# Performance work log

Measured on AMD Instinct MI355X. Metric: run time of the kernel, lower is better.

The kernel has to match this reference:

```python
import jax, jax.numpy as jnp
import numpy as np
from functools import partial

EMB = 768
ATTN = 768
HEADS = 12
N = 4096
K = 64
ALPHA = 0.5
TEMP = 0.5
THRESH = 1e-4
MAX_ITER = 100
DKM_EPS = 1e-6
LN_EPS = 1e-5


def setup_inputs() -> dict:
    key = jax.random.key(0)
    ks = jax.random.split(key, 12)
    s = 0.02
    return {
        "original_embeddings": jax.random.normal(ks[0], (N, EMB), jnp.float32),
        "fc1_w": jax.random.normal(ks[1], (ATTN, EMB), jnp.float32) * s,
        "fc1_b": jnp.zeros((ATTN,), jnp.float32),
        "fc2_w": jax.random.normal(ks[2], (EMB, ATTN), jnp.float32) * s,
        "fc2_b": jnp.zeros((EMB,), jnp.float32),
        "in_proj_w": jax.random.normal(ks[3], (3 * ATTN, ATTN), jnp.float32) * s,
        "in_proj_b": jnp.zeros((3 * ATTN,), jnp.float32),
        "out_w": jax.random.normal(ks[4], (ATTN, ATTN), jnp.float32) * s,
        "out_b": jnp.zeros((ATTN,), jnp.float32),
        "ln_g": jnp.ones((EMB,), jnp.float32),
        "ln_b": jnp.zeros((EMB,), jnp.float32),
        "init_idx": jax.random.randint(ks[5], (K,), 0, N, jnp.int64 if jax.config.jax_enable_x64 else jnp.int32),
        "k_cl": K,
    }


def _cdist(x, c):
    # squared euclidean via expansion, clipped for numerical safety
    sq = (jnp.sum(x * x, 1)[:, None] + jnp.sum(c * c, 1)[None, :]
          - 2.0 * (x @ c.T))
    return jnp.sqrt(jnp.maximum(sq, 0.0))


def _dkm_step(X, C):
    a = jax.nn.softmax(-_cdist(X, C) / TEMP, axis=1)   # [N, K]
    a_sum = jnp.sum(a, axis=0) + DKM_EPS               # [K]
    C_new = (a.T @ X) / a_sum[:, None]                 # [K, D]
    return a, C_new


def _transform(x, fc1_w, fc1_b, fc2_w, fc2_b, in_proj_w, in_proj_b, out_w, out_b, ln_g, ln_b):
    h = jax.nn.relu(x @ fc1_w.T + fc1_b)               # [N, A]
    qkv = h @ in_proj_w.T + in_proj_b                  # [N, 3A]
    q, k, v = jnp.split(qkv, 3, axis=1)
    hd = ATTN // HEADS
    q = q.reshape(N, HEADS, hd).transpose(1, 0, 2)     # [H, N, hd]
    k = k.reshape(N, HEADS, hd).transpose(1, 0, 2)
    v = v.reshape(N, HEADS, hd).transpose(1, 0, 2)
    scores = jnp.einsum('hnd,hmd->hnm', q, k) / np.sqrt(hd).astype(np.float32)
    attn = jax.nn.softmax(scores, axis=-1)             # [H, N, N]
    o = jnp.einsum('hnm,hmd->hnd', attn, v)            # [H, N, hd]
    o = o.transpose(1, 0, 2).reshape(N, ATTN)
    o = o @ out_w.T + out_b
    y = jax.nn.relu(o @ fc2_w.T + fc2_b)               # [N, E]
    z = (1.0 - ALPHA) * x + ALPHA * y
    mu = jnp.mean(z, axis=-1, keepdims=True)
    var = jnp.mean((z - mu) ** 2, axis=-1, keepdims=True)
    return (z - mu) / jnp.sqrt(var + LN_EPS) * ln_g + ln_b


def reference(original_embeddings, fc1_w, fc1_b, fc2_w, fc2_b,
              in_proj_w, in_proj_b, out_w, out_b, ln_g, ln_b,
              init_idx, k_cl):
    X = _transform(original_embeddings, fc1_w, fc1_b, fc2_w, fc2_b,
                   in_proj_w, in_proj_b, out_w, out_b, ln_g, ln_b)
    C0 = X[init_idx]                                   # [K, E]
    a0, C1 = _dkm_step(X, C0)
    diff0 = jnp.sum(jnp.abs(C1 - C0))

    def cond(st):
        _, _, _, diff, i = st
        return (diff > THRESH) & (i < MAX_ITER)

    def body(st):
        _, _, C_new, _, i = st
        C = C_new
        a, C_new2 = _dkm_step(X, C)
        diff = jnp.sum(jnp.abs(C_new2 - C))
        return (C, a, C_new2, diff, i + 1)

    C, a, _, _, _ = jax.lax.while_loop(cond, body, (C0, a0, C1, diff0, jnp.int32(0)))
    return C, a
```

## Files before the change

kernel.cpp:

```cpp
#include <hip/hip_runtime.h>
#include <cstdint>

typedef __bf16 bf16;
typedef __bf16 bf16x4 __attribute__((ext_vector_type(4)));
typedef __bf16 bf16x8 __attribute__((ext_vector_type(8)));
typedef float  f32x4  __attribute__((ext_vector_type(4)));

#define LOG2E 1.44269504088896340736f

__device__ __forceinline__ f32x4 mfma16(bf16x8 a, bf16x8 b, f32x4 c) {
  return __builtin_amdgcn_mfma_f32_16x16x32_bf16(a, b, c, 0, 0, 0);
}

__device__ __forceinline__ void gl2lds16(const bf16* g, bf16* l) {
  __builtin_amdgcn_global_load_lds(
      (const __attribute__((address_space(1))) unsigned int*)g,
      (__attribute__((address_space(3))) unsigned int*)l, 16, 0, 0);
}

__global__ __launch_bounds__(256) void cvt_all(
    const float* __restrict__ x0, const float* __restrict__ w1,
    const float* __restrict__ w2, const float* __restrict__ wip,
    const float* __restrict__ wo,
    bf16* __restrict__ dx0, bf16* __restrict__ dw1, bf16* __restrict__ dw2,
    bf16* __restrict__ dwip, bf16* __restrict__ dwo, float* __restrict__ ctrl)
{
  int i = blockIdx.x * 256 + threadIdx.x;
  if (blockIdx.x == 0) {
    for (int u = threadIdx.x; u < 8192; u += 256) ctrl[u] = 0.f;
  }
  const float* s; bf16* d; int base;
  if      (i <  786432) { s = x0;  d = dx0;  base = 0; }
  else if (i <  933888) { s = w1;  d = dw1;  base = 786432; }
  else if (i < 1081344) { s = w2;  d = dw2;  base = 933888; }
  else if (i < 1523712) { s = wip; d = dwip; base = 1081344; }
  else                  { s = wo;  d = dwo;  base = 1523712; }
  int j = i - base;
  f32x4 v = ((const f32x4*)s)[j];
  bf16x4 r;
  r[0] = (bf16)v[0]; r[1] = (bf16)v[1]; r[2] = (bf16)v[2]; r[3] = (bf16)v[3];
  ((bf16x4*)d)[j] = r;
}

__global__ __launch_bounds__(256) void bias_fuse(
    const float* __restrict__ w2, const float* __restrict__ bo,
    const float* __restrict__ b2, float* __restrict__ bc)
{
  const int w = threadIdx.x >> 6, lane = threadIdx.x & 63;
  const int n = blockIdx.x * 4 + w;
  float s = 0.f;
#pragma unroll
  for (int i = 0; i < 12; ++i) {
    int col = lane + i * 64;
    s += w2[(size_t)n * 768 + col] * bo[col];
  }
#pragma unroll
  for (int off = 32; off; off >>= 1) s += __shfl_xor(s, off, 64);
  if (lane == 0) bc[n] = b2[n] + s;
}

template<int RELU, int OUTF32>
__global__ __launch_bounds__(256) void gemm128(
    const bf16* __restrict__ A, const bf16* __restrict__ W,
    const float* __restrict__ bias, bf16* __restrict__ outb,
    float* __restrict__ outf, int N)
{
  __shared__ bf16 Ab[2][8192];
  __shared__ bf16 Bb[2][8192];
  const int tid = threadIdx.x;
  const int w = tid >> 6, lane = tid & 63;
  const int q2 = lane >> 4, c = lane & 15;
  const int wrow = (w >> 1) * 64, wcol = (w & 1) * 64;
  const int mb = blockIdx.x * 128, nb = blockIdx.y * 128;
  const int srow = tid >> 3, sgrp = tid & 7;

  auto stage = [&](const bf16* __restrict__ src, int rowbase, int kb, bf16* dst) {
#pragma unroll
    for (int i = 0; i < 4; ++i) {
      int row = i * 32 + srow;
      int gs = (sgrp ^ (row & 7)) * 8;
      gl2lds16(src + (size_t)(rowbase + row) * 768 + kb + gs,
               dst + i * 2048 + tid * 8);
    }
  };

  f32x4 acc[4][4] = {};
  stage(A, mb, 0, Ab[0]);
  stage(W, nb, 0, Bb[0]);
  for (int kb = 0; kb < 12; ++kb) {
    const int buf = kb & 1;
    __syncthreads();
    if (kb < 11) {
      stage(A, mb, (kb + 1) * 64, Ab[buf ^ 1]);
      stage(W, nb, (kb + 1) * 64, Bb[buf ^ 1]);
    }
#pragma unroll
    for (int kc = 0; kc < 2; ++kc) {
      bf16x8 af[4], bfr[4];
#pragma unroll
      for (int rt = 0; rt < 4; ++rt) {
        int r = wrow + rt * 16 + c;
        af[rt] = *(const bf16x8*)&Ab[buf][r * 64 + (((kc * 4 + q2) ^ (r & 7)) * 8)];
      }
#pragma unroll
      for (int ct = 0; ct < 4; ++ct) {
        int r = wcol + ct * 16 + c;
        bfr[ct] = *(const bf16x8*)&Bb[buf][r * 64 + (((kc * 4 + q2) ^ (r & 7)) * 8)];
      }
#pragma unroll
      for (int rt = 0; rt < 4; ++rt)
#pragma unroll
        for (int ct = 0; ct < 4; ++ct)
          acc[rt][ct] = mfma16(af[rt], bfr[ct], acc[rt][ct]);
    }
  }
#pragma unroll
  for (int rt = 0; rt < 4; ++rt) {
#pragma unroll
    for (int ct = 0; ct < 4; ++ct) {
      int col = nb + wcol + ct * 16 + c;
      float bv = bias[col];
#pragma unroll
      for (int j = 0; j < 4; ++j) {
        int row = mb + wrow + rt * 16 + q2 * 4 + j;
        float v = acc[rt][ct][j] + bv;
        if (RELU) v = fmaxf(v, 0.f);
        if (OUTF32) outf[(size_t)row * N + col] = v;
        else        outb[(size_t)row * N + col] = (bf16)v;
      }
    }
  }
}

__global__ __launch_bounds__(256) void transpose_bf16(
    const bf16* __restrict__ src, bf16* __restrict__ dst,
    int stride, int colOff, int dstride)
{
  __shared__ bf16 t[64][72];
  const int br = blockIdx.x, bc = blockIdx.y;
  {
    int ir = threadIdx.x >> 2, icb = (threadIdx.x & 3) * 16;
    const bf16* srow = src + (size_t)(br * 64 + ir) * stride + colOff + bc * 64 + icb;
    *(bf16x8*)&t[ir][icb] = *(const bf16x8*)srow;
    *(bf16x8*)&t[ir][icb + 8] = *(const bf16x8*)(srow + 8);
  }
  __syncthreads();
  {
    int oc = threadIdx.x >> 2, orb = (threadIdx.x & 3) * 16;
    bf16x8 v0, v1;
#pragma unroll
    for (int j = 0; j < 8; ++j) { v0[j] = t[orb + j][oc]; v1[j] = t[orb + 8 + j][oc]; }
    bf16* drow = dst + (size_t)(bc * 64 + oc) * dstride + br * 64 + orb;
    *(bf16x8*)drow = v0;
    *(bf16x8*)(drow + 8) = v1;
  }
}

__global__ __launch_bounds__(256) void attn_kernel(
    const bf16* __restrict__ qkv, const bf16* __restrict__ vt, bf16* __restrict__ o)
{
  const int h = blockIdx.x >> 6;
  const int qt = blockIdx.x & 63;
  const int w = threadIdx.x >> 6, lane = threadIdx.x & 63;
  const int q2 = lane >> 4, c = lane & 15;
  const int qbase = qt * 64 + w * 16;
  __shared__ bf16 Ks[2][64][64];
  __shared__ bf16 Vs[2][64][64];
  __shared__ bf16 Pl[4][16][72];

  const bf16* Qr = qkv + (size_t)(qbase + c) * 2304 + h * 64 + q2 * 8;
  bf16x8 a0 = *(const bf16x8*)(Qr);
  bf16x8 a1 = *(const bf16x8*)(Qr + 32);

  const int srow = lane >> 3;
  const int sg = ((lane & 7) ^ srow) * 8;
  const bf16* kg = qkv + (size_t)(w * 16 + srow) * 2304 + 768 + h * 64 + sg;
  const bf16* vg = vt + (size_t)(h * 64 + w * 16 + srow) * 4096 + sg;

  auto stage = [&](int jt, int buf) {
    const int kvb = jt * 64;
    gl2lds16(kg + (size_t)kvb * 2304,       &Ks[buf][w * 16][0]);
    gl2lds16(kg + (size_t)(kvb + 8) * 2304, &Ks[buf][w * 16 + 8][0]);
    gl2lds16(vg + kvb,                      &Vs[buf][w * 16][0]);
    gl2lds16(vg + kvb + 8 * 4096,           &Vs[buf][w * 16 + 8][0]);
  };

  bf16x8 ones;
#pragma unroll
  for (int i = 0; i < 8; ++i) ones[i] = (bf16)1.0f;

  f32x4 oa[4] = {};
  f32x4 accl = {};
  const int gsw = (q2 ^ (c & 7)) * 8;
  const float SC = 0.125f * LOG2E;

  stage(0, 0);
  for (int jt = 0; jt < 64; ++jt) {
    const int buf = jt & 1;
    __syncthreads();
    if (jt < 63) stage(jt + 1, buf ^ 1);
    f32x4 s[4];
#pragma unroll
    for (int nt = 0; nt < 4; ++nt) {
      const int row = nt * 16 + c;
      bf16x8 b0 = *(const bf16x8*)&Ks[buf][row][gsw];
      bf16x8 b1 = *(const bf16x8*)&Ks[buf][row][gsw ^ 32];
      f32x4 t = {};
      t = mfma16(a0, b0, t);
      t = mfma16(a1, b1, t);
      s[nt] = t;
    }
#pragma unroll
    for (int nt = 0; nt < 4; ++nt)
#pragma unroll
      for (int j = 0; j < 4; ++j)
        Pl[w][q2 * 4 + j][nt * 16 + c] = (bf16)exp2f(s[nt][j] * SC);
    bf16x8 p0 = *(const bf16x8*)(&Pl[w][c][q2 * 8]);
    bf16x8 p1 = *(const bf16x8*)(&Pl[w][c][32 + q2 * 8]);
    accl = mfma16(p0, ones, accl);
    accl = mfma16(p1, ones, accl);
#pragma unroll
    for (int dt = 0; dt < 4; ++dt) {
      const int row = dt * 16 + c;
      bf16x8 v0 = *(const bf16x8*)&Vs[buf][row][gsw];
      bf16x8 v1 = *(const bf16x8*)&Vs[buf][row][gsw ^ 32];
      oa[dt] = mfma16(p0, v0, oa[dt]);
      oa[dt] = mfma16(p1, v1, oa[dt]);
    }
  }
#pragma unroll
  for (int dt = 0; dt < 4; ++dt)
#pragma unroll
    for (int j = 0; j < 4; ++j) {
      int row = qbase + q2 * 4 + j;
      int col = h * 64 + dt * 16 + c;
      o[(size_t)row * 768 + col] = (bf16)(oa[dt][j] / accl[j]);
    }
}

__global__ __launch_bounds__(256) void ln_kernel(
    const float* __restrict__ x0, const float* __restrict__ y,
    const float* __restrict__ g, const float* __restrict__ b,
    float* __restrict__ X, bf16* __restrict__ Xb, float* __restrict__ xn2)
{
  const int w = threadIdx.x >> 6, lane = threadIdx.x & 63;
  const int row = blockIdx.x * 4 + w;
  const float* xr = x0 + (size_t)row * 768;
  const float* yr = y + (size_t)row * 768;
  float z[12]; float s = 0.f;
#pragma unroll
  for (int i = 0; i < 12; ++i) {
    int col = lane + i * 64;
    float zz = 0.5f * xr[col] + 0.5f * yr[col];
    z[i] = zz; s += zz;
  }
#pragma unroll
  for (int off = 32; off; off >>= 1) s += __shfl_xor(s, off, 64);
  float mu = s * (1.f / 768.f);
  float v = 0.f;
#pragma unroll
  for (int i = 0; i < 12; ++i) { float d = z[i] - mu; v += d * d; }
#pragma unroll
  for (int off = 32; off; off >>= 1) v += __shfl_xor(v, off, 64);
  float rstd = rsqrtf(v * (1.f / 768.f) + 1e-5f);
  float sn = 0.f;
#pragma unroll
  for (int i = 0; i < 12; ++i) {
    int col = lane + i * 64;
    float xv = (z[i] - mu) * rstd * g[col] + b[col];
    X[(size_t)row * 768 + col] = xv;
    Xb[(size_t)row * 768 + col] = (bf16)xv;
    sn += xv * xv;
  }
#pragma unroll
  for (int off = 32; off; off >>= 1) sn += __shfl_xor(sn, off, 64);
  if (lane == 0) xn2[row] = sn;
}

__device__ __forceinline__ void gridbar(int* bar, int& ep, int g) {
  __syncthreads();
  if (threadIdx.x == 0) {
    ep++;
    __builtin_amdgcn_fence(__ATOMIC_RELEASE, "agent");
    int v = __hip_atomic_fetch_add(bar + g * 64, 1, __ATOMIC_RELAXED,
                                   __HIP_MEMORY_SCOPE_AGENT) + 1;
    if (v == 32 * ep) {
      int tv = __hip_atomic_fetch_add(bar + 512, 1, __ATOMIC_RELAXED,
                                      __HIP_MEMORY_SCOPE_AGENT) + 1;
      if (tv == 8 * ep) {
#pragma unroll
        for (int i = 0; i < 8; ++i)
          __hip_atomic_store(bar + 1024 + i * 64, ep, __ATOMIC_RELAXED,
                             __HIP_MEMORY_SCOPE_AGENT);
      }
    }
    long guard = 0;
    while (__hip_atomic_load(bar + 1024 + g * 64, __ATOMIC_RELAXED,
                             __HIP_MEMORY_SCOPE_AGENT) < ep) {
      __builtin_amdgcn_s_sleep(2);
      if (++guard > (1L << 28)) break;
    }
    __builtin_amdgcn_fence(__ATOMIC_ACQUIRE, "agent");
  }
  __syncthreads();
}

__global__ __launch_bounds__(256) void dkm_fused(
    const float* __restrict__ XF, const int* __restrict__ idx,
    const bf16* __restrict__ Xb, const bf16* __restrict__ Xt,
    const float* __restrict__ xn2,
    float* __restrict__ CB, bf16* __restrict__ CBH,
    bf16* __restrict__ aT, float* __restrict__ a_out, float* __restrict__ outC,
    float* __restrict__ asumall, float* __restrict__ cnall,
    float* __restrict__ diffall, int* __restrict__ bar)
{
  extern __shared__ char dynsmem[];
  bf16* XtL = (bf16*)dynsmem;
  __shared__ bf16 XL[16][776];
  __shared__ float GsRed[1024];
  __shared__ float asl[64];
  __shared__ float cnl[16];
  __shared__ float dred[4];
  __shared__ float sdiff;
  float (*Gs)[64] = (float(*)[64])GsRed;
  float (*red)[16][16] = (float(*)[16][16])GsRed;
  const int tid = threadIdx.x;
  const int w = tid >> 6, lane = tid & 63;
  const int q2 = lane >> 4, c = lane & 15;
  const int b = blockIdx.x;
  const int g = b & 7;
  const int rbase = b * 16;
  const int tr = b / 48, tc = b % 48;
  int ep = 0;

  {
    int row = tid >> 4, seg = (tid & 15) * 48;
    const bf16* src = Xb + (size_t)(rbase + row) * 768 + seg;
#pragma unroll
    for (int i = 0; i < 6; ++i)
      *(bf16x8*)&XL[row][seg + i * 8] = *(const bf16x8*)(src + i * 8);
  }
  if (b < 192) {
    const int row = tid >> 4, cc = tid & 15;
    const bf16* XtS = Xt + (size_t)(tc * 16 + row) * 4096;
#pragma unroll
    for (int i = 0; i < 32; ++i) {
      int gg = i * 16 + cc;
      bf16x8 vv = *(const bf16x8*)(XtS + gg * 8);
      *(bf16x8*)&XtL[(size_t)row * 4096 + ((gg ^ (row & 7)) * 8)] = vv;
    }
  }
  if (b < 64) {
    const int src = idx[b];
    float s = 0.f;
#pragma unroll
    for (int u = 0; u < 3; ++u) {
      int d = u * 256 + tid;
      float v = XF[(size_t)src * 768 + d];
      CB[(size_t)b * 768 + d] = v;
      CBH[(size_t)b * 768 + d] = (bf16)v;
      s += v * v;
    }
#pragma unroll
    for (int off = 32; off; off >>= 1) s += __shfl_xor(s, off, 64);
    if (lane == 0) dred[w] = s;
    __syncthreads();
    if (tid == 0) cnall[b] = dred[0] + dred[1] + dred[2] + dred[3];
  }
  const int arow = tid >> 4, aci = tid & 15;
  const float xn = xn2[rbase + arow];
  gridbar(bar, ep, g);

  int p = 0;
  for (int t = 0; t < 100; ++t) {
    const int par = t & 1;
    {
      if (b == 0) {
        if (tid >= 128 && tid < 192) asumall[(par ^ 1) * 64 + tid - 128] = 0.f;
        else if (tid >= 192)         cnall[(par ^ 1) * 64 + tid - 192] = 0.f;
      }
      const bf16* C = CBH + (size_t)par * 49152;
      const float* cnp = cnall + par * 64;
      const bf16* Cr = C + (size_t)(w * 16 + c) * 768 + q2 * 8;
      f32x4 a0 = {}, a1 = {}, a2 = {}, a3 = {};
#pragma unroll
      for (int ks = 0; ks < 24; ks += 4) {
        a0 = mfma16(*(const bf16x8*)&XL[c][q2 * 8 + ks * 32],
                    *(const bf16x8*)(Cr + ks * 32), a0);
        a1 = mfma16(*(const bf16x8*)&XL[c][q2 * 8 + (ks + 1) * 32],
                    *(const bf16x8*)(Cr + (ks + 1) * 32), a1);
        a2 = mfma16(*(const bf16x8*)&XL[c][q2 * 8 + (ks + 2) * 32],
                    *(const bf16x8*)(Cr + (ks + 2) * 32), a2);
        a3 = mfma16(*(const bf16x8*)&XL[c][q2 * 8 + (ks + 3) * 32],
                    *(const bf16x8*)(Cr + (ks + 3) * 32), a3);
      }
      f32x4 acc = (a0 + a1) + (a2 + a3);
      if (tid < 64) asl[tid] = 0.f;
#pragma unroll
      for (int j = 0; j < 4; ++j) Gs[q2 * 4 + j][w * 16 + c] = acc[j];
      __syncthreads();
      float lg[4];
#pragma unroll
      for (int u = 0; u < 4; ++u) {
        int col = aci + u * 16;
        float d2 = xn + cnp[col] - 2.f * Gs[arow][col];
        lg[u] = -2.f * sqrtf(fmaxf(d2, 0.f));
      }
      float mx = fmaxf(fmaxf(lg[0], lg[1]), fmaxf(lg[2], lg[3]));
#pragma unroll
      for (int off = 8; off; off >>= 1) mx = fmaxf(mx, __shfl_xor(mx, off, 16));
      float sum = 0.f;
#pragma unroll
      for (int u = 0; u < 4; ++u) { float e = exp2f((lg[u] - mx) * LOG2E); lg[u] = e; sum += e; }
#pragma unroll
      for (int off = 8; off; off >>= 1) sum += __shfl_xor(sum, off, 16);
      float rs = 1.f / sum;
#pragma unroll
      for (int u = 0; u < 4; ++u) {
        int col = aci + u * 16;
        float av = lg[u] * rs;
        aT[(size_t)col * 4096 + rbase + arow] = (bf16)av;
        atomicAdd(&asl[col], av);
      }
      __syncthreads();
      if (tid < 64) atomicAdd(&asumall[par * 64 + tid], asl[tid]);
    }
    gridbar(bar, ep, g);
    if (b < 192) {
      const bf16* Ar = aT + (size_t)(tr * 16 + c) * 4096 + q2 * 8;
      f32x4 b0 = {}, b1 = {}, b2 = {}, b3 = {};
#pragma unroll
      for (int i = 0; i < 32; i += 4) {
#pragma unroll
        for (int u = 0; u < 4; ++u) {
          int ii = i + u;
          int kb = (w + ii * 4) * 32;
          int gb = (w + ii * 4) * 4 + q2;
          bf16x8 bv = *(const bf16x8*)&XtL[(size_t)c * 4096 + ((gb ^ (c & 7)) * 8)];
          bf16x8 av = *(const bf16x8*)(Ar + kb);
          if (u == 0) b0 = mfma16(av, bv, b0);
          else if (u == 1) b1 = mfma16(av, bv, b1);
          else if (u == 2) b2 = mfma16(av, bv, b2);
          else b3 = mfma16(av, bv, b3);
        }
      }
      f32x4 acc = (b0 + b1) + (b2 + b3);
#pragma unroll
      for (int j = 0; j < 4; ++j) red[w][q2 * 4 + j][c] = acc[j];
      if (tid < 16) cnl[tid] = 0.f;
      __syncthreads();
      const int r = tid >> 4, cl = tid & 15;
      float s = red[0][r][cl] + red[1][r][cl] + red[2][r][cl] + red[3][r][cl];
      const int cluster = tr * 16 + r, dcol = tc * 16 + cl;
      float denom = asumall[par * 64 + cluster] + 1e-6f;
      float cnew = s / denom;
      size_t cidx = (size_t)cluster * 768 + dcol;
      float cold = CB[(size_t)par * 49152 + cidx];
      CB[(size_t)(par ^ 1) * 49152 + cidx] = cnew;
      CBH[(size_t)(par ^ 1) * 49152 + cidx] = (bf16)cnew;
      atomicAdd(&cnl[r], cnew * cnew);
      float dv = fabsf(cnew - cold);
#pragma unroll
      for (int off = 32; off; off >>= 1) dv += __shfl_xor(dv, off, 64);
      if (lane == 0) dred[w] = dv;
      __syncthreads();
      if (tid < 16)
        atomicAdd(&cnall[(par ^ 1) * 64 + tr * 16 + tid], cnl[tid]);
      if (tid == 0)
        atomicAdd(&diffall[par], dred[0] + dred[1] + dred[2] + dred[3]);
    } else if (b == 255 && tid == 0) {
      diffall[par ^ 1] = 0.f;
    }
    gridbar(bar, ep, g);
    if (tid == 0)
      sdiff = *(volatile const float*)&diffall[par];
    __syncthreads();
    if (sdiff <= 1e-4f) { p = par; break; }
    p = (t + 1) & 1;
  }
  {
    const bf16* C = CBH + (size_t)p * 49152;
    const float* cnp = cnall + p * 64;
    f32x4 acc = {};
    const bf16* Cr = C + (size_t)(w * 16 + c) * 768 + q2 * 8;
#pragma unroll
    for (int ks = 0; ks < 24; ++ks) {
      bf16x8 a = *(const bf16x8*)&XL[c][q2 * 8 + ks * 32];
      bf16x8 bb = *(const bf16x8*)(Cr + ks * 32);
      acc = mfma16(a, bb, acc);
    }
    __syncthreads();
#pragma unroll
    for (int j = 0; j < 4; ++j) Gs[q2 * 4 + j][w * 16 + c] = acc[j];
    __syncthreads();
    float lg[4];
#pragma unroll
    for (int u = 0; u < 4; ++u) {
      int col = aci + u * 16;
      float d2 = xn + cnp[col] - 2.f * Gs[arow][col];
      lg[u] = -2.f * sqrtf(fmaxf(d2, 0.f));
    }
    float mx = fmaxf(fmaxf(lg[0], lg[1]), fmaxf(lg[2], lg[3]));
#pragma unroll
    for (int off = 8; off; off >>= 1) mx = fmaxf(mx, __shfl_xor(mx, off, 16));
    float sum = 0.f;
#pragma unroll
    for (int u = 0; u < 4; ++u) { float e = exp2f((lg[u] - mx) * LOG2E); lg[u] = e; sum += e; }
#pragma unroll
    for (int off = 8; off; off >>= 1) sum += __shfl_xor(sum, off, 16);
    float rs = 1.f / sum;
#pragma unroll
    for (int u = 0; u < 4; ++u)
      a_out[(size_t)(rbase + arow) * 64 + aci + u * 16] = lg[u] * rs;
  }
  if (tid < 192) outC[b * 192 + tid] = CB[(size_t)p * 49152 + b * 192 + tid];
}

extern "C" void kernel_launch(void* const* d_in, const int* in_sizes, int n_in,
                              void* d_out, int out_size, void* d_ws, size_t ws_size,
                              hipStream_t stream) {
  const float* x0   = (const float*)d_in[0];
  const float* fc1w = (const float*)d_in[1];
  const float* fc1b = (const float*)d_in[2];
  const float* fc2w = (const float*)d_in[3];
  const float* fc2b = (const float*)d_in[4];
  const float* ipw  = (const float*)d_in[5];
  const float* ipb  = (const float*)d_in[6];
  const float* outw = (const float*)d_in[7];
  const float* outbias = (const float*)d_in[8];
  const float* lng  = (const float*)d_in[9];
  const float* lnb  = (const float*)d_in[10];
  const int*   idx  = (const int*)d_in[11];

  char* p = (char*)d_ws;
  auto take = [&](size_t n) { char* r = p; p += (n + 255) & ~(size_t)255; return r; };
  bf16* X0B   = (bf16*)take((size_t)4096 * 768 * 2);
  bf16* W1B   = (bf16*)take((size_t)768 * 768 * 2);
  bf16* FC2WB = (bf16*)take((size_t)768 * 768 * 2);
  bf16* IPWB  = (bf16*)take((size_t)2304 * 768 * 2);
  bf16* OUTWB = (bf16*)take((size_t)768 * 768 * 2);
  bf16* WOT   = (bf16*)take((size_t)768 * 768 * 2);
  bf16* WCB   = (bf16*)take((size_t)768 * 768 * 2);
  float* BC   = (float*)take(768 * 4);
  bf16* HB    = (bf16*)take((size_t)4096 * 768 * 2);
  bf16* QKVB  = (bf16*)take((size_t)4096 * 2304 * 2);
  bf16* VT    = (bf16*)take((size_t)768 * 4096 * 2);
  bf16* OB    = (bf16*)take((size_t)4096 * 768 * 2);
  float* YF   = (float*)take((size_t)4096 * 768 * 4);
  float* XF   = (float*)take((size_t)4096 * 768 * 4);
  bf16* XBB   = (bf16*)take((size_t)4096 * 768 * 2);
  bf16* XTB   = (bf16*)take((size_t)768 * 4096 * 2);
  float* XN2  = (float*)take((size_t)4096 * 4);
  float* CB   = (float*)take((size_t)2 * 49152 * 4);
  bf16* CBH   = (bf16*)take((size_t)2 * 49152 * 2);
  bf16* ATB   = (bf16*)take((size_t)64 * 4096 * 2);
  float* CTRLF = (float*)take(8192 * 4);
  float* ASUM = CTRLF;
  float* CN   = CTRLF + 128;
  float* DIFF = CTRLF + 256;
  int* BAR    = (int*)(CTRLF + 512);
  float* ZB   = CTRLF + 4096;

  float* aout = (float*)d_out + 49152;

  cvt_all<<<6528, 256, 0, stream>>>(x0, fc1w, fc2w, ipw, outw,
                                    X0B, W1B, FC2WB, IPWB, OUTWB, CTRLF);
  transpose_bf16<<<dim3(12, 12), 256, 0, stream>>>(OUTWB, WOT, 768, 0, 768);
  bias_fuse<<<192, 256, 0, stream>>>(fc2w, outbias, fc2b, BC);
  gemm128<0, 0><<<dim3(6, 6), 256, 0, stream>>>(FC2WB, WOT, ZB, WCB, nullptr, 768);

  gemm128<1, 0><<<dim3(32, 6), 256, 0, stream>>>(X0B, W1B, fc1b, HB, nullptr, 768);
  gemm128<0, 0><<<dim3(32, 18), 256, 0, stream>>>(HB, IPWB, ipb, QKVB, nullptr, 2304);
  transpose_bf16<<<dim3(64, 12), 256, 0, stream>>>(QKVB, VT, 2304, 1536, 4096);
  attn_kernel<<<768, 256, 0, stream>>>(QKVB, VT, OB);
  gemm128<1, 1><<<dim3(32, 6), 256, 0, stream>>>(OB, WCB, BC, nullptr, YF, 768);
  ln_kernel<<<1024, 256, 0, stream>>>(x0, YF, lng, lnb, XF, XBB, XN2);
  transpose_bf16<<<dim3(64, 12), 256, 0, stream>>>(XBB, XTB, 768, 0, 4096);
  dkm_fused<<<256, 256, 131072, stream>>>(XF, idx, XBB, XTB, XN2, CB, CBH, ATB, aout,
                                          (float*)d_out, ASUM, CN, DIFF, BAR);
}
```

Measured before the change: 551.5 us.

## Split DKM blocks into assignment and centroid roles and drop precomputed weight fusion

The persistent DKM kernel now uses 224 blocks. 128 of them compute soft assignments over 32 rows each. The other 96 hold a transposed 16-column slice of X in LDS, built directly from Xb with scattered stores, and each updates two 16-cluster centroid tiles. The global-barrier group count changes to match. The out_proj·fc2 weight pre-fusion (transpose, bias_fuse, fused GEMM) and the separate X transpose kernel are removed in favour of two plain GEMMs, trading fewer launches for an extra GEMM and a less balanced role split.

```diff
diff --git a/kernel.cpp b/kernel.cpp
--- a/kernel.cpp
+++ b/kernel.cpp
@@ -40,23 +40,6 @@
   bf16x4 r;
   r[0] = (bf16)v[0]; r[1] = (bf16)v[1]; r[2] = (bf16)v[2]; r[3] = (bf16)v[3];
   ((bf16x4*)d)[j] = r;
-}
-
-__global__ __launch_bounds__(256) void bias_fuse(
-    const float* __restrict__ w2, const float* __restrict__ bo,
-    const float* __restrict__ b2, float* __restrict__ bc)
-{
-  const int w = threadIdx.x >> 6, lane = threadIdx.x & 63;
-  const int n = blockIdx.x * 4 + w;
-  float s = 0.f;
-#pragma unroll
-  for (int i = 0; i < 12; ++i) {
-    int col = lane + i * 64;
-    s += w2[(size_t)n * 768 + col] * bo[col];
-  }
-#pragma unroll
-  for (int off = 32; off; off >>= 1) s += __shfl_xor(s, off, 64);
-  if (lane == 0) bc[n] = b2[n] + s;
 }
 
 template<int RELU, int OUTF32>
@@ -284,7 +267,7 @@
     __builtin_amdgcn_fence(__ATOMIC_RELEASE, "agent");
     int v = __hip_atomic_fetch_add(bar + g * 64, 1, __ATOMIC_RELAXED,
                                    __HIP_MEMORY_SCOPE_AGENT) + 1;
-    if (v == 32 * ep) {
+    if (v == 28 * ep) {
       int tv = __hip_atomic_fetch_add(bar + 512, 1, __ATOMIC_RELAXED,
                                       __HIP_MEMORY_SCOPE_AGENT) + 1;
       if (tv == 8 * ep) {
@@ -307,47 +290,50 @@
 
 __global__ __launch_bounds__(256) void dkm_fused(
     const float* __restrict__ XF, const int* __restrict__ idx,
-    const bf16* __restrict__ Xb, const bf16* __restrict__ Xt,
-    const float* __restrict__ xn2,
+    const bf16* __restrict__ Xb, const float* __restrict__ xn2,
     float* __restrict__ CB, bf16* __restrict__ CBH,
     bf16* __restrict__ aT, float* __restrict__ a_out, float* __restrict__ outC,
     float* __restrict__ asumall, float* __restrict__ cnall,
     float* __restrict__ diffall, int* __restrict__ bar)
 {
   extern __shared__ char dynsmem[];
-  bf16* XtL = (bf16*)dynsmem;
-  __shared__ bf16 XL[16][776];
-  __shared__ float GsRed[1024];
+  __shared__ float GsRed[32 * 68];
   __shared__ float asl[64];
   __shared__ float cnl[16];
   __shared__ float dred[4];
   __shared__ float sdiff;
-  float (*Gs)[64] = (float(*)[64])GsRed;
+  float (*Gs)[68] = (float(*)[68])GsRed;
   float (*red)[16][16] = (float(*)[16][16])GsRed;
   const int tid = threadIdx.x;
   const int w = tid >> 6, lane = tid & 63;
   const int q2 = lane >> 4, c = lane & 15;
   const int b = blockIdx.x;
   const int g = b & 7;
-  const int rbase = b * 16;
-  const int tr = b / 48, tc = b % 48;
+  const bool isA = (b >= 96);
+  const int tcs = b >> 1;
+  const int trh = (b & 1) * 2;
+  const int rbase = (b - 96) * 32;
   int ep = 0;
 
-  {
-    int row = tid >> 4, seg = (tid & 15) * 48;
+  bf16* XL  = (bf16*)dynsmem;
+  bf16* XtL = (bf16*)dynsmem;
+
+  if (isA) {
+    int row = tid >> 3, seg = (tid & 7) * 96;
     const bf16* src = Xb + (size_t)(rbase + row) * 768 + seg;
 #pragma unroll
-    for (int i = 0; i < 6; ++i)
-      *(bf16x8*)&XL[row][seg + i * 8] = *(const bf16x8*)(src + i * 8);
-  }
-  if (b < 192) {
-    const int row = tid >> 4, cc = tid & 15;
-    const bf16* XtS = Xt + (size_t)(tc * 16 + row) * 4096;
-#pragma unroll
+    for (int i = 0; i < 12; ++i)
+      *(bf16x8*)&XL[row * 776 + seg + i * 8] = *(const bf16x8*)(src + i * 8);
+  } else {
+    const int h = tid & 1;
     for (int i = 0; i < 32; ++i) {
-      int gg = i * 16 + cc;
-      bf16x8 vv = *(const bf16x8*)(XtS + gg * 8);
-      *(bf16x8*)&XtL[(size_t)row * 4096 + ((gg ^ (row & 7)) * 8)] = vv;
+      int n = i * 128 + (tid >> 1);
+      bf16x8 v = *(const bf16x8*)(Xb + (size_t)n * 768 + tcs * 16 + h * 8);
+#pragma unroll
+      for (int e = 0; e < 8; ++e) {
+        int dcol = h * 8 + e;
+        XtL[(size_t)dcol * 4096 + (((n >> 3) ^ (dcol & 7)) * 8) + (n & 7)] = v[e];
+      }
     }
   }
   if (b < 64) {
@@ -367,108 +353,117 @@
     __syncthreads();
     if (tid == 0) cnall[b] = dred[0] + dred[1] + dred[2] + dred[3];
   }
-  const int arow = tid >> 4, aci = tid & 15;
-  const float xn = xn2[rbase + arow];
+  const int arow = tid >> 3, asub = tid & 7;
+  const float xn = isA ? xn2[rbase + arow] : 0.f;
   gridbar(bar, ep, g);
 
   int p = 0;
   for (int t = 0; t < 100; ++t) {
     const int par = t & 1;
-    {
-      if (b == 0) {
-        if (tid >= 128 && tid < 192) asumall[(par ^ 1) * 64 + tid - 128] = 0.f;
-        else if (tid >= 192)         cnall[(par ^ 1) * 64 + tid - 192] = 0.f;
-      }
-      const bf16* C = CBH + (size_t)par * 49152;
+    if (isA) {
+      const bf16* Cc = CBH + (size_t)par * 49152;
       const float* cnp = cnall + par * 64;
-      const bf16* Cr = C + (size_t)(w * 16 + c) * 768 + q2 * 8;
-      f32x4 a0 = {}, a1 = {}, a2 = {}, a3 = {};
-#pragma unroll
-      for (int ks = 0; ks < 24; ks += 4) {
-        a0 = mfma16(*(const bf16x8*)&XL[c][q2 * 8 + ks * 32],
-                    *(const bf16x8*)(Cr + ks * 32), a0);
-        a1 = mfma16(*(const bf16x8*)&XL[c][q2 * 8 + (ks + 1) * 32],
-                    *(const bf16x8*)(Cr + (ks + 1) * 32), a1);
-        a2 = mfma16(*(const bf16x8*)&XL[c][q2 * 8 + (ks + 2) * 32],
-                    *(const bf16x8*)(Cr + (ks + 2) * 32), a2);
-        a3 = mfma16(*(const bf16x8*)&XL[c][q2 * 8 + (ks + 3) * 32],
-                    *(const bf16x8*)(Cr + (ks + 3) * 32), a3);
-      }
-      f32x4 acc = (a0 + a1) + (a2 + a3);
+      const bf16* Cr = Cc + (size_t)(w * 16 + c) * 768 + q2 * 8;
+      const bf16* X0r = XL + (size_t)c * 776 + q2 * 8;
+      const bf16* X1r = XL + (size_t)(16 + c) * 776 + q2 * 8;
+      f32x4 g00 = {}, g01 = {}, g10 = {}, g11 = {};
+#pragma unroll
+      for (int ks = 0; ks < 24; ks += 2) {
+        bf16x8 b0 = *(const bf16x8*)(Cr + ks * 32);
+        bf16x8 b1 = *(const bf16x8*)(Cr + (ks + 1) * 32);
+        g00 = mfma16(*(const bf16x8*)(X0r + ks * 32), b0, g00);
+        g10 = mfma16(*(const bf16x8*)(X1r + ks * 32), b0, g10);
+        g01 = mfma16(*(const bf16x8*)(X0r + (ks + 1) * 32), b1, g01);
+        g11 = mfma16(*(const bf16x8*)(X1r + (ks + 1) * 32), b1, g11);
+      }
+      f32x4 acc0 = g00 + g01, acc1 = g10 + g11;
       if (tid < 64) asl[tid] = 0.f;
 #pragma unroll
-      for (int j = 0; j < 4; ++j) Gs[q2 * 4 + j][w * 16 + c] = acc[j];
+      for (int j = 0; j < 4; ++j) {
+        Gs[q2 * 4 + j][w * 16 + c] = acc0[j];
+        Gs[16 + q2 * 4 + j][w * 16 + c] = acc1[j];
+      }
       __syncthreads();
-      float lg[4];
-#pragma unroll
-      for (int u = 0; u < 4; ++u) {
-        int col = aci + u * 16;
+      float lg[8];
+#pragma unroll
+      for (int u = 0; u < 8; ++u) {
+        int col = asub + u * 8;
         float d2 = xn + cnp[col] - 2.f * Gs[arow][col];
         lg[u] = -2.f * sqrtf(fmaxf(d2, 0.f));
       }
-      float mx = fmaxf(fmaxf(lg[0], lg[1]), fmaxf(lg[2], lg[3]));
-#pragma unroll
-      for (int off = 8; off; off >>= 1) mx = fmaxf(mx, __shfl_xor(mx, off, 16));
+      float mx = lg[0];
+#pragma unroll
+      for (int u = 1; u < 8; ++u) mx = fmaxf(mx, lg[u]);
+#pragma unroll
+      for (int off = 4; off; off >>= 1) mx = fmaxf(mx, __shfl_xor(mx, off, 8));
       float sum = 0.f;
 #pragma unroll
-      for (int u = 0; u < 4; ++u) { float e = exp2f((lg[u] - mx) * LOG2E); lg[u] = e; sum += e; }
-#pragma unroll
-      for (int off = 8; off; off >>= 1) sum += __shfl_xor(sum, off, 16);
+      for (int u = 0; u < 8; ++u) { float e = exp2f((lg[u] - mx) * LOG2E); lg[u] = e; sum += e; }
+#pragma unroll
+      for (int off = 4; off; off >>= 1) sum += __shfl_xor(sum, off, 8);
       float rs = 1.f / sum;
 #pragma unroll
-      for (int u = 0; u < 4; ++u) {
-        int col = aci + u * 16;
+      for (int u = 0; u < 8; ++u) {
+        int col = asub + u * 8;
         float av = lg[u] * rs;
         aT[(size_t)col * 4096 + rbase + arow] = (bf16)av;
         atomicAdd(&asl[col], av);
       }
       __syncthreads();
       if (tid < 64) atomicAdd(&asumall[par * 64 + tid], asl[tid]);
+    } else if (b == 0) {
+      if (tid >= 128 && tid < 192) asumall[(par ^ 1) * 64 + tid - 128] = 0.f;
+      else if (tid >= 192)         cnall[(par ^ 1) * 64 + tid - 192] = 0.f;
     }
     gridbar(bar, ep, g);
-    if (b < 192) {
-      const bf16* Ar = aT + (size_t)(tr * 16 + c) * 4096 + q2 * 8;
-      f32x4 b0 = {}, b1 = {}, b2 = {}, b3 = {};
-#pragma unroll
-      for (int i = 0; i < 32; i += 4) {
-#pragma unroll
-        for (int u = 0; u < 4; ++u) {
-          int ii = i + u;
-          int kb = (w + ii * 4) * 32;
-          int gb = (w + ii * 4) * 4 + q2;
-          bf16x8 bv = *(const bf16x8*)&XtL[(size_t)c * 4096 + ((gb ^ (c & 7)) * 8)];
-          bf16x8 av = *(const bf16x8*)(Ar + kb);
-          if (u == 0) b0 = mfma16(av, bv, b0);
-          else if (u == 1) b1 = mfma16(av, bv, b1);
-          else if (u == 2) b2 = mfma16(av, bv, b2);
-          else b3 = mfma16(av, bv, b3);
+    if (!isA) {
+#pragma unroll 1
+      for (int ti = 0; ti < 2; ++ti) {
+        const int tr = trh + ti;
+        const bf16* Ar = aT + (size_t)(tr * 16 + c) * 4096 + q2 * 8;
+        f32x4 b0 = {}, b1 = {}, b2 = {}, b3 = {};
+#pragma unroll
+        for (int i = 0; i < 32; i += 4) {
+#pragma unroll
+          for (int u = 0; u < 4; ++u) {
+            int ii = i + u;
+            int kb = (w + ii * 4) * 32;
+            int gb = (w + ii * 4) * 4 + q2;
+            bf16x8 bv = *(const bf16x8*)&XtL[(size_t)c * 4096 + ((gb ^ (c & 7)) * 8)];
+            bf16x8 av = *(const bf16x8*)(Ar + kb);
+            if (u == 0) b0 = mfma16(av, bv, b0);
+            else if (u == 1) b1 = mfma16(av, bv, b1);
+            else if (u == 2) b2 = mfma16(av, bv, b2);
+            else b3 = mfma16(av, bv, b3);
+          }
         }
-      }
-      f32x4 acc = (b0 + b1) + (b2 + b3);
-#pragma unroll
-      for (int j = 0; j < 4; ++j) red[w][q2 * 4 + j][c] = acc[j];
-      if (tid < 16) cnl[tid] = 0.f;
-      __syncthreads();
-      const int r = tid >> 4, cl = tid & 15;
-      float s = red[0][r][cl] + red[1][r][cl] + red[2][r][cl] + red[3][r][cl];
-      const int cluster = tr * 16 + r, dcol = tc * 16 + cl;
-      float denom = asumall[par * 64 + cluster] + 1e-6f;
-      float cnew = s / denom;
-      size_t cidx = (size_t)cluster * 768 + dcol;
-      float cold = CB[(size_t)par * 49152 + cidx];
-      CB[(size_t)(par ^ 1) * 49152 + cidx] = cnew;
-      CBH[(size_t)(par ^ 1) * 49152 + cidx] = (bf16)cnew;
-      atomicAdd(&cnl[r], cnew * cnew);
-      float dv = fabsf(cnew - cold);
-#pragma unroll
-      for (int off = 32; off; off >>= 1) dv += __shfl_xor(dv, off, 64);
-      if (lane == 0) dred[w] = dv;
-      __syncthreads();
-      if (tid < 16)
-        atomicAdd(&cnall[(par ^ 1) * 64 + tr * 16 + tid], cnl[tid]);
-      if (tid == 0)
-        atomicAdd(&diffall[par], dred[0] + dred[1] + dred[2] + dred[3]);
-    } else if (b == 255 && tid == 0) {
+        f32x4 acc = (b0 + b1) + (b2 + b3);
+        __syncthreads();
+#pragma unroll
+        for (int j = 0; j < 4; ++j) red[w][q2 * 4 + j][c] = acc[j];
+        if (tid < 16) cnl[tid] = 0.f;
+        __syncthreads();
+        const int r = tid >> 4, cl = tid & 15;
+        float s = red[0][r][cl] + red[1][r][cl] + red[2][r][cl] + red[3][r][cl];
+        const int cluster = tr * 16 + r, dcol = tcs * 16 + cl;
+        float denom = asumall[par * 64 + cluster] + 1e-6f;
+        float cnew = s / denom;
+        size_t cidx = (size_t)cluster * 768 + dcol;
+        float cold = CB[(size_t)par * 49152 + cidx];
+        CB[(size_t)(par ^ 1) * 49152 + cidx] = cnew;
+        CBH[(size_t)(par ^ 1) * 49152 + cidx] = (bf16)cnew;
+        atomicAdd(&cnl[r], cnew * cnew);
+        float dv = fabsf(cnew - cold);
+#pragma unroll
+        for (int off = 32; off; off >>= 1) dv += __shfl_xor(dv, off, 64);
+        if (lane == 0) dred[w] = dv;
+        __syncthreads();
+        if (tid < 16)
+          atomicAdd(&cnall[(par ^ 1) * 64 + tr * 16 + tid], cnl[tid]);
+        if (tid == 0)
+          atomicAdd(&diffall[par], dred[0] + dred[1] + dred[2] + dred[3]);
+      }
+    } else if (b == 223 && tid == 0) {
       diffall[par ^ 1] = 0.f;
     }
     gridbar(bar, ep, g);
@@ -478,42 +473,52 @@
     if (sdiff <= 1e-4f) { p = par; break; }
     p = (t + 1) & 1;
   }
-  {
-    const bf16* C = CBH + (size_t)p * 49152;
+  if (isA) {
+    const bf16* Cc = CBH + (size_t)p * 49152;
     const float* cnp = cnall + p * 64;
-    f32x4 acc = {};
-    const bf16* Cr = C + (size_t)(w * 16 + c) * 768 + q2 * 8;
+    const bf16* Cr = Cc + (size_t)(w * 16 + c) * 768 + q2 * 8;
+    const bf16* X0r = XL + (size_t)c * 776 + q2 * 8;
+    const bf16* X1r = XL + (size_t)(16 + c) * 776 + q2 * 8;
+    f32x4 acc0 = {}, acc1 = {};
 #pragma unroll
     for (int ks = 0; ks < 24; ++ks) {
-      bf16x8 a = *(const bf16x8*)&XL[c][q2 * 8 + ks * 32];
       bf16x8 bb = *(const bf16x8*)(Cr + ks * 32);
-      acc = mfma16(a, bb, acc);
+      acc0 = mfma16(*(const bf16x8*)(X0r + ks * 32), bb, acc0);
+      acc1 = mfma16(*(const bf16x8*)(X1r + ks * 32), bb, acc1);
     }
     __syncthreads();
 #pragma unroll
-    for (int j = 0; j < 4; ++j) Gs[q2 * 4 + j][w * 16 + c] = acc[j];
+    for (int j = 0; j < 4; ++j) {
+      Gs[q2 * 4 + j][w * 16 + c] = acc0[j];
+      Gs[16 + q2 * 4 + j][w * 16 + c] = acc1[j];
+    }
     __syncthreads();
-    float lg[4];
-#pragma unroll
-    for (int u = 0; u < 4; ++u) {
-      int col = aci + u * 16;
+    float lg[8];
+#pragma unroll
+    for (int u = 0; u < 8; ++u) {
+      int col = asub + u * 8;
       float d2 = xn + cnp[col] - 2.f * Gs[arow][col];
       lg[u] = -2.f * sqrtf(fmaxf(d2, 0.f));
     }
-    float mx = fmaxf(fmaxf(lg[0], lg[1]), fmaxf(lg[2], lg[3]));
-#pragma unroll
-    for (int off = 8; off; off >>= 1) mx = fmaxf(mx, __shfl_xor(mx, off, 16));
+    float mx = lg[0];
+#pragma unroll
+    for (int u = 1; u < 8; ++u) mx = fmaxf(mx, lg[u]);
+#pragma unroll
+    for (int off = 4; off; off >>= 1) mx = fmaxf(mx, __shfl_xor(mx, off, 8));
     float sum = 0.f;
 #pragma unroll
-    for (int u = 0; u < 4; ++u) { float e = exp2f((lg[u] - mx) * LOG2E); lg[u] = e; sum += e; }
-#pragma unroll
-    for (int off = 8; off; off >>= 1) sum += __shfl_xor(sum, off, 16);
+    for (int u = 0; u < 8; ++u) { float e = exp2f((lg[u] - mx) * LOG2E); lg[u] = e; sum += e; }
+#pragma unroll
+    for (int off = 4; off; off >>= 1) sum += __shfl_xor(sum, off, 8);
     float rs = 1.f / sum;
 #pragma unroll
-    for (int u = 0; u < 4; ++u)
-      a_out[(size_t)(rbase + arow) * 64 + aci + u * 16] = lg[u] * rs;
-  }
-  if (tid < 192) outC[b * 192 + tid] = CB[(size_t)p * 49152 + b * 192 + tid];
+    for (int u = 0; u < 8; ++u)
+      a_out[(size_t)(rbase + arow) * 64 + asub + u * 8] = lg[u] * rs;
+  }
+  {
+    int i = b * 220 + tid;
+    if (tid < 220 && i < 49152) outC[i] = CB[(size_t)p * 49152 + i];
+  }
 }
 
 extern "C" void kernel_launch(void* const* d_in, const int* in_sizes, int n_in,
@@ -539,17 +544,14 @@
   bf16* FC2WB = (bf16*)take((size_t)768 * 768 * 2);
   bf16* IPWB  = (bf16*)take((size_t)2304 * 768 * 2);
   bf16* OUTWB = (bf16*)take((size_t)768 * 768 * 2);
-  bf16* WOT   = (bf16*)take((size_t)768 * 768 * 2);
-  bf16* WCB   = (bf16*)take((size_t)768 * 768 * 2);
-  float* BC   = (float*)take(768 * 4);
   bf16* HB    = (bf16*)take((size_t)4096 * 768 * 2);
   bf16* QKVB  = (bf16*)take((size_t)4096 * 2304 * 2);
   bf16* VT    = (bf16*)take((size_t)768 * 4096 * 2);
   bf16* OB    = (bf16*)take((size_t)4096 * 768 * 2);
+  bf16* O2B   = (bf16*)take((size_t)4096 * 768 * 2);
   float* YF   = (float*)take((size_t)4096 * 768 * 4);
   float* XF   = (float*)take((size_t)4096 * 768 * 4);
   bf16* XBB   = (bf16*)take((size_t)4096 * 768 * 2);
-  bf16* XTB   = (bf16*)take((size_t)768 * 4096 * 2);
   float* XN2  = (float*)take((size_t)4096 * 4);
   float* CB   = (float*)take((size_t)2 * 49152 * 4);
   bf16* CBH   = (bf16*)take((size_t)2 * 49152 * 2);
@@ -559,23 +561,18 @@
   float* CN   = CTRLF + 128;
   float* DIFF = CTRLF + 256;
   int* BAR    = (int*)(CTRLF + 512);
-  float* ZB   = CTRLF + 4096;
 
   float* aout = (float*)d_out + 49152;
 
   cvt_all<<<6528, 256, 0, stream>>>(x0, fc1w, fc2w, ipw, outw,
                                     X0B, W1B, FC2WB, IPWB, OUTWB, CTRLF);
-  transpose_bf16<<<dim3(12, 12), 256, 0, stream>>>(OUTWB, WOT, 768, 0, 768);
-  bias_fuse<<<192, 256, 0, stream>>>(fc2w, outbias, fc2b, BC);
-  gemm128<0, 0><<<dim3(6, 6), 256, 0, stream>>>(FC2WB, WOT, ZB, WCB, nullptr, 768);
-
   gemm128<1, 0><<<dim3(32, 6), 256, 0, stream>>>(X0B, W1B, fc1b, HB, nullptr, 768);
   gemm128<0, 0><<<dim3(32, 18), 256, 0, stream>>>(HB, IPWB, ipb, QKVB, nullptr, 2304);
   transpose_bf16<<<dim3(64, 12), 256, 0, stream>>>(QKVB, VT, 2304, 1536, 4096);
   attn_kernel<<<768, 256, 0, stream>>>(QKVB, VT, OB);
-  gemm128<1, 1><<<dim3(32, 6), 256, 0, stream>>>(OB, WCB, BC, nullptr, YF, 768);
+  gemm128<0, 0><<<dim3(32, 6), 256, 0, stream>>>(OB, OUTWB, outbias, O2B, nullptr, 768);
+  gemm128<1, 1><<<dim3(32, 6), 256, 0, stream>>>(O2B, FC2WB, fc2b, nullptr, YF, 768);
   ln_kernel<<<1024, 256, 0, stream>>>(x0, YF, lng, lnb, XF, XBB, XN2);
-  transpose_bf16<<<dim3(64, 12), 256, 0, stream>>>(XBB, XTB, 768, 0, 4096);
-  dkm_fused<<<256, 256, 131072, stream>>>(XF, idx, XBB, XTB, XN2, CB, CBH, ATB, aout,
+  dkm_fused<<<224, 256, 131072, stream>>>(XF, idx, XBB, XN2, CB, CBH, ATB, aout,
                                           (float*)d_out, ASUM, CN, DIFF, BAR);
 }
```

After: 682.7 us. 23.8% more time.
